# Kernel tuning notes

Measured on AMD Instinct MI355X. Metric: run time of the kernel, lower is better.

Reference implementation:

```python
import jax, jax.numpy as jnp
import numpy as np

N = 100000       # num nodes
E = 3200000      # train message edges (avg degree 32)
EP = 1600000     # pos (and neg) decode edges
F_IN = 128       # node feature dim
H1, H2 = 50, 10  # GCN layer widths from source


def setup_inputs() -> dict:
    key = jax.random.key(0)
    ks = jax.random.split(key, 6)
    x = jax.random.normal(ks[0], (N, F_IN), dtype=jnp.float32)
    train_pos_edge_index = jax.random.randint(ks[1], (2, E), 0, N)
    pos_edge_index = jax.random.randint(ks[2], (2, EP), 0, N)
    neg_edge_index = jax.random.randint(ks[3], (2, EP), 0, N)
    W1 = jax.random.normal(ks[4], (F_IN, H1), dtype=jnp.float32) / np.float32(np.sqrt(F_IN))
    b1 = jnp.zeros((H1,), jnp.float32)
    W2 = jax.random.normal(ks[5], (H1, H2), dtype=jnp.float32) / np.float32(np.sqrt(H1))
    b2 = jnp.zeros((H2,), jnp.float32)
    return {"x": x, "W1": W1, "b1": b1, "W2": W2, "b2": b2,
            "train_pos_edge_index": train_pos_edge_index,
            "pos_edge_index": pos_edge_index,
            "neg_edge_index": neg_edge_index}


def gcn_conv(x, W, b, src, dst, num_nodes):
    # x: [N, Fin] -> transform first (PyG GCNConv), then normalize+aggregate.
    h = x @ W                                                        # [N, Fout]
    deg = jax.ops.segment_sum(jnp.ones(src.shape, h.dtype), dst,
                              num_segments=num_nodes)                # in-degree incl self-loops
    dinv = jnp.where(deg > 0, jax.lax.rsqrt(deg), 0.0)
    norm = dinv[src] * dinv[dst]                                     # [E']
    msgs = h[src] * norm[:, None]                                    # gather + scale
    out = jax.ops.segment_sum(msgs, dst, num_segments=num_nodes)     # scatter-add
    return out + b


def reference(x, W1, b1, W2, b2, train_pos_edge_index, pos_edge_index, neg_edge_index):
    # GCNConv adds self-loops to the message edge set.
    loops = jnp.arange(N, dtype=train_pos_edge_index.dtype)
    src = jnp.concatenate([train_pos_edge_index[0], loops])
    dst = jnp.concatenate([train_pos_edge_index[1], loops])
    # encode(): conv1 -> relu -> conv2
    h = jax.nn.relu(gcn_conv(x, W1, b1, src, dst, N))                # [N, 50]
    z = gcn_conv(h, W2, b2, src, dst, N)                             # [N, 10]
    # decode(): concat pos/neg edges, edge-wise dot product of endpoint embeddings
    ei = jnp.concatenate([pos_edge_index, neg_edge_index], axis=-1)  # [2, 2*EP]
    logits = jnp.sum(z[ei[0]] * z[ei[1]], axis=-1)                   # [2*EP]
    return logits
```

## Files before the change

kernel.cpp:

```cpp
#include <hip/hip_runtime.h>

#define FIN 128
#define H1_ 50
#define H2_ 10

#define BKT_SHIFT 7
#define BKT_W 128
#define NB_MAX 800
#define P1_CHUNK 8192


__device__ inline float bf2f(unsigned int u16) {
    union { unsigned int i; float f; } c; c.i = u16 << 16; return c.f;
}
__device__ inline unsigned short f2bf(float f) {
    union { float f; unsigned int i; } c; c.f = f;
    unsigned int x = c.i;
    return (unsigned short)((x + 0x7FFFu + ((x >> 16) & 1u)) >> 16);
}


__global__ __launch_bounds__(256) void bucket_count(const int* __restrict__ dst,
                                                    int* __restrict__ bcnt, int E) {
    __shared__ int lh[NB_MAX];
    int tid = threadIdx.x;
    for (int i = tid; i < NB_MAX; i += 256) lh[i] = 0;
    __syncthreads();
    int lo = blockIdx.x * P1_CHUNK;
    int hi = min(lo + P1_CHUNK, E);
    for (int e = lo + tid; e < hi; e += 256)
        atomicAdd(&lh[dst[e] >> BKT_SHIFT], 1);
    __syncthreads();
    for (int b = tid; b < NB_MAX; b += 256) {
        int c = lh[b];
        if (c) atomicAdd(&bcnt[b], c);
    }
}

__global__ __launch_bounds__(256) void bucket_scan(const int* __restrict__ bcnt,
                                                   int* __restrict__ bbase,
                                                   int* __restrict__ bcursor,
                                                   int nb2, int E) {
    __shared__ int s[256];
    int t = threadIdx.x;
    int base = t * 4;
    int v0 = (base + 0 < nb2) ? bcnt[base + 0] : 0;
    int v1 = (base + 1 < nb2) ? bcnt[base + 1] : 0;
    int v2 = (base + 2 < nb2) ? bcnt[base + 2] : 0;
    int v3 = (base + 3 < nb2) ? bcnt[base + 3] : 0;
    int tsum = v0 + v1 + v2 + v3;
    s[t] = tsum;
    __syncthreads();
    for (int off = 1; off < 256; off <<= 1) {
        int x = (t >= off) ? s[t - off] : 0;
        __syncthreads();
        s[t] += x;
        __syncthreads();
    }
    int excl = s[t] - tsum;
    if (t == 0) bbase[nb2] = E;
    if (base + 0 < nb2) { bbase[base + 0] = excl; bcursor[base + 0] = excl; }
    excl += v0;
    if (base + 1 < nb2) { bbase[base + 1] = excl; bcursor[base + 1] = excl; }
    excl += v1;
    if (base + 2 < nb2) { bbase[base + 2] = excl; bcursor[base + 2] = excl; }
    excl += v2;
    if (base + 3 < nb2) { bbase[base + 3] = excl; bcursor[base + 3] = excl; }
}


__global__ __launch_bounds__(256) void partition_pass1(const int* __restrict__ src,
                                                       const int* __restrict__ dst,
                                                       int* __restrict__ bcursor,
                                                       int* __restrict__ pairbuf, int E) {
    __shared__ int lhist[NB_MAX];
    __shared__ int lbase[NB_MAX];
    int tid = threadIdx.x;
    for (int i = tid; i < NB_MAX; i += 256) lhist[i] = 0;
    __syncthreads();
    int lo = blockIdx.x * P1_CHUNK;
    int hi = min(lo + P1_CHUNK, E);
    for (int e = lo + tid; e < hi; e += 256)
        atomicAdd(&lhist[dst[e] >> BKT_SHIFT], 1);
    __syncthreads();
    for (int b = tid; b < NB_MAX; b += 256) {
        int c = lhist[b];
        lbase[b] = c ? atomicAdd(&bcursor[b], c) : 0;
    }
    __syncthreads();
    for (int i = tid; i < NB_MAX; i += 256) lhist[i] = 0;
    __syncthreads();
    for (int e = lo + tid; e < hi; e += 256) {
        int s = src[e], d = dst[e];
        int b = d >> BKT_SHIFT;
        int r = atomicAdd(&lhist[b], 1);
        pairbuf[lbase[b] + r] = s | ((d & (BKT_W - 1)) << 17);
    }
}


__global__ __launch_bounds__(256) void bucket_fill_scan(const int* __restrict__ pairbuf,
                                                        const int* __restrict__ bbase,
                                                        int* __restrict__ rowptr,
                                                        float* __restrict__ dinv,
                                                        int* __restrict__ ecol,
                                                        int N, int E) {
    __shared__ int cnt[BKT_W];
    __shared__ int sc[BKT_W];
    __shared__ int cur[BKT_W];
    int b = blockIdx.x;
    int base_node = b << BKT_SHIFT;
    int nnodes = min(BKT_W, N - base_node);
    int tid = threadIdx.x;
    if (tid < BKT_W) cnt[tid] = 0;
    __syncthreads();
    int lo = bbase[b], hi = bbase[b + 1];
    for (int j = lo + tid; j < hi; j += 256)
        atomicAdd(&cnt[pairbuf[j] >> 17], 1);
    __syncthreads();
    int c = (tid < BKT_W) ? cnt[tid] : 0;
    if (tid < BKT_W) sc[tid] = c;
    __syncthreads();
    for (int off = 1; off < BKT_W; off <<= 1) {
        int xv = (tid >= off && tid < BKT_W) ? sc[tid - off] : 0;
        __syncthreads();
        if (tid < BKT_W) sc[tid] += xv;
        __syncthreads();
    }
    if (tid < nnodes) {
        int rp = lo + sc[tid] - c;
        rowptr[base_node + tid] = rp;
        cur[tid] = rp;
        dinv[base_node + tid] = rsqrtf(1.0f + (float)c);
    }
    __syncthreads();
    for (int j = lo + tid; j < hi; j += 256) {
        int p = pairbuf[j];
        int pos = atomicAdd(&cur[p >> 17], 1);
        ecol[pos] = p & 0x1FFFF;
    }
    if (b == (int)gridDim.x - 1 && tid == 0) rowptr[N] = E;
}


#define G1_NODES 32
#define SX_PITCH 132
__global__ __launch_bounds__(256) void gemm1_kernel(const float* __restrict__ x,
                                                    const float* __restrict__ W1,
                                                    const float* __restrict__ dinv,
                                                    unsigned short* __restrict__ st1p, int N) {
    __shared__ float sW[FIN * 64];
    __shared__ float sX[G1_NODES * SX_PITCH];
    int tid = threadIdx.x;
    int nb = blockIdx.x * G1_NODES;
    for (int i = tid; i < FIN * 64; i += 256) {
        int k = i >> 6, f = i & 63;
        sW[i] = (f < H1_) ? W1[k * H1_ + f] : 0.0f;
    }
    {
        const float4* x4 = (const float4*)(x + (size_t)nb * FIN);
        for (int i = tid; i < G1_NODES * 32; i += 256) {
            int ln = i >> 5, kk = i & 31;
            float4 v = (nb + ln < N) ? x4[(size_t)ln * 32 + kk]
                                     : make_float4(0.f, 0.f, 0.f, 0.f);
            *(float4*)(&sX[ln * SX_PITCH + kk * 4]) = v;
        }
    }
    __syncthreads();
    int ln = tid >> 3;
    int g  = tid & 7;
    int node = nb + ln;
    const float* xr = &sX[ln * SX_PITCH];
    const float* wc = &sW[g * 8];
    float acc[8] = {0, 0, 0, 0, 0, 0, 0, 0};
#pragma unroll 4
    for (int k = 0; k < FIN; ++k) {
        float xv = xr[k];
        const float* w = &wc[k * 64];
#pragma unroll
        for (int j = 0; j < 8; ++j) acc[j] = fmaf(xv, w[j], acc[j]);
    }
    if (node >= N) return;
    float di = dinv[node];
    unsigned short o[8];
#pragma unroll
    for (int j = 0; j < 8; ++j) o[j] = f2bf(acc[j] * di);
    uint4 pk;
    pk.x = (unsigned)o[0] | ((unsigned)o[1] << 16);
    pk.y = (unsigned)o[2] | ((unsigned)o[3] << 16);
    pk.z = (unsigned)o[4] | ((unsigned)o[5] << 16);
    pk.w = (unsigned)o[6] | ((unsigned)o[7] << 16);
    *(uint4*)(st1p + (size_t)node * 64 + g * 8) = pk;
}


#define F2 25
__global__ __launch_bounds__(256) void csr_aggregate1(const unsigned short* __restrict__ st,
                                                      const int* __restrict__ rowptr,
                                                      const int* __restrict__ ecol,
                                                      const float* __restrict__ dinv,
                                                      const float* __restrict__ b,
                                                      float* __restrict__ out, int N) {
    int idx = blockIdx.x * blockDim.x + threadIdx.x;
    if (idx >= N * F2) return;
    int d  = idx / F2;
    int fp = idx - d * F2;
    int fo = 2 * fp;
    unsigned int self2 = *(const unsigned int*)(st + (size_t)d * 64 + fo);
    float acc0 = bf2f(self2 & 0xFFFFu);
    float acc1 = bf2f(self2 >> 16);
    int j = rowptr[d], end = rowptr[d + 1];
    for (; j + 3 < end; j += 4) {
        int s0 = ecol[j], s1 = ecol[j + 1], s2 = ecol[j + 2], s3 = ecol[j + 3];
        unsigned int v0 = *(const unsigned int*)(st + (size_t)s0 * 64 + fo);
        unsigned int v1 = *(const unsigned int*)(st + (size_t)s1 * 64 + fo);
        unsigned int v2 = *(const unsigned int*)(st + (size_t)s2 * 64 + fo);
        unsigned int v3 = *(const unsigned int*)(st + (size_t)s3 * 64 + fo);
        acc0 += (bf2f(v0 & 0xFFFFu) + bf2f(v1 & 0xFFFFu)) + (bf2f(v2 & 0xFFFFu) + bf2f(v3 & 0xFFFFu));
        acc1 += (bf2f(v0 >> 16) + bf2f(v1 >> 16)) + (bf2f(v2 >> 16) + bf2f(v3 >> 16));
    }
    for (; j < end; ++j) {
        unsigned int v = *(const unsigned int*)(st + (size_t)ecol[j] * 64 + fo);
        acc0 += bf2f(v & 0xFFFFu);
        acc1 += bf2f(v >> 16);
    }
    float vd = dinv[d];
    float r0 = fmaxf(fmaf(vd, acc0, b[fo]),     0.0f);
    float r1 = fmaxf(fmaf(vd, acc1, b[fo + 1]), 0.0f);
    *(float2*)(out + (size_t)d * H1_ + fo) = make_float2(r0, r1);
}


__global__ __launch_bounds__(256) void gemm2_kernel(const float* __restrict__ h,
                                                    const float* __restrict__ W2,
                                                    const float* __restrict__ dinv,
                                                    float* __restrict__ st2, int n) {
    __shared__ float sW[H1_ * H2_];
    int tid = threadIdx.x;
    for (int i = tid; i < H1_ * H2_; i += 256) sW[i] = W2[i];
    __syncthreads();
    int idx = blockIdx.x * blockDim.x + tid;
    if (idx >= n) return;
    int node = idx / H2_;
    int f    = idx - node * H2_;
    const float* hr = &h[node * H1_];
    float acc = 0.0f;
#pragma unroll
    for (int k = 0; k < H1_; ++k) acc = fmaf(hr[k], sW[k * H2_ + f], acc);
    st2[idx] = acc * dinv[node];
}


template <int F, bool RELU>
__global__ __launch_bounds__(256) void csr_aggregate(const float* __restrict__ st,
                                                     const int* __restrict__ rowptr,
                                                     const int* __restrict__ ecol,
                                                     const float* __restrict__ dinv,
                                                     const float* __restrict__ b,
                                                     float* __restrict__ out, int N) {
    int idx = blockIdx.x * blockDim.x + threadIdx.x;
    if (idx >= N * F) return;
    int d = idx / F;
    int f = idx - d * F;
    float acc = st[idx];
    int j = rowptr[d], end = rowptr[d + 1];
    for (; j + 3 < end; j += 4) {
        int s0 = ecol[j], s1 = ecol[j + 1], s2 = ecol[j + 2], s3 = ecol[j + 3];
        float a0 = st[s0 * F + f], a1 = st[s1 * F + f];
        float a2 = st[s2 * F + f], a3 = st[s3 * F + f];
        acc += (a0 + a1) + (a2 + a3);
    }
    for (; j < end; ++j) acc += st[ecol[j] * F + f];
    float v = fmaf(dinv[d], acc, b[f]);
    out[idx] = RELU ? fmaxf(v, 0.0f) : v;
}


__global__ void decode_kernel(const float* __restrict__ z, const int* __restrict__ pos,
                              const int* __restrict__ neg, float* __restrict__ logits, int EP) {
    int i = blockIdx.x * blockDim.x + threadIdx.x;
    if (i >= 2 * EP) return;
    int a, b;
    if (i < EP) { a = pos[i]; b = pos[EP + i]; }
    else        { int j = i - EP; a = neg[j]; b = neg[EP + j]; }
    const float* za = &z[a * H2_];
    const float* zb = &z[b * H2_];
    float acc = 0.0f;
#pragma unroll
    for (int f = 0; f < H2_; ++f) acc = fmaf(za[f], zb[f], acc);
    logits[i] = acc;
}


extern "C" void kernel_launch(void* const* d_in, const int* in_sizes, int n_in,
                              void* d_out, int out_size, void* d_ws, size_t ws_size,
                              hipStream_t stream) {
    const float* x   = (const float*)d_in[0];
    const float* W1  = (const float*)d_in[1];
    const float* b1  = (const float*)d_in[2];
    const float* W2  = (const float*)d_in[3];
    const float* b2  = (const float*)d_in[4];
    const int* train = (const int*)d_in[5];
    const int* pos   = (const int*)d_in[6];
    const int* neg   = (const int*)d_in[7];

    const int N  = in_sizes[0] / FIN;
    const int E  = in_sizes[5] / 2;
    const int EP = in_sizes[6] / 2;

    const int* tsrc = train;
    const int* tdst = train + E;

    size_t off = 0;
    int* rowptr   = (int*)d_ws;              off += (size_t)N + 1;
    int* bcnt     = (int*)d_ws + off;        off += NB_MAX;
    int* bbase    = (int*)d_ws + off;        off += NB_MAX + 1;
    int* bcursor  = (int*)d_ws + off;        off += NB_MAX;
    float* dinv   = (float*)d_ws + off;      off += N;
    off = (off + 3) & ~(size_t)3;
    float* regA   = (float*)d_ws + off;      off += (size_t)32 * N;
    float* regB   = (float*)d_ws + off;
    unsigned short* st1p = (unsigned short*)regA;
    float* st2    = regA;
    float* out2   = regA + (size_t)10 * N;
    float* out1   = regB;
    int* pairbuf  = (int*)regB;
    int* ecol     = (int*)d_out;
    float* logits = (float*)d_out;

    const int NB2 = (N + BKT_W - 1) >> BKT_SHIFT;
    const int P1B = (E + P1_CHUNK - 1) / P1_CHUNK;

    hipMemsetAsync(bcnt, 0, NB_MAX * sizeof(int), stream);
    bucket_count<<<P1B, 256, 0, stream>>>(tdst, bcnt, E);
    bucket_scan<<<1, 256, 0, stream>>>(bcnt, bbase, bcursor, NB2, E);
    partition_pass1<<<P1B, 256, 0, stream>>>(tsrc, tdst, bcursor, pairbuf, E);
    bucket_fill_scan<<<NB2, 256, 0, stream>>>(pairbuf, bbase, rowptr, dinv, ecol, N, E);

    gemm1_kernel<<<(N + G1_NODES - 1) / G1_NODES, 256, 0, stream>>>(x, W1, dinv, st1p, N);
    csr_aggregate1<<<(N * F2 + 255) / 256, 256, 0, stream>>>(
        st1p, rowptr, ecol, dinv, b1, out1, N);

    gemm2_kernel<<<(N * H2_ + 255) / 256, 256, 0, stream>>>(out1, W2, dinv, st2, N * H2_);
    csr_aggregate<H2_, false><<<(N * H2_ + 255) / 256, 256, 0, stream>>>(
        st2, rowptr, ecol, dinv, b2, out2, N);

    decode_kernel<<<(2 * EP + 255) / 256, 256, 0, stream>>>(out2, pos, neg, logits, EP);
}
```

Baseline: 476.4 us.

## Split edge partition into two-level radix pass via superbuckets

```diff
diff --git a/kernel.cpp b/kernel.cpp
--- a/kernel.cpp
+++ b/kernel.cpp
@@ -7,7 +7,11 @@
 #define BKT_SHIFT 7
 #define BKT_W 128
 #define NB_MAX 800
+#define SB_SHIFT 11
+#define SB_W 2048
+#define NSB_MAX 64
 #define P1_CHUNK 8192
+#define P1F_CHUNK 4096
 
 
 __device__ inline float bf2f(unsigned int u16) {
@@ -40,7 +44,9 @@
 __global__ __launch_bounds__(256) void bucket_scan(const int* __restrict__ bcnt,
                                                    int* __restrict__ bbase,
                                                    int* __restrict__ bcursor,
-                                                   int nb2, int E) {
+                                                   int* __restrict__ sbbase,
+                                                   int* __restrict__ sbcursor,
+                                                   int nb2, int nsb, int E) {
     __shared__ int s[256];
     int t = threadIdx.x;
     int base = t * 4;
@@ -66,35 +72,74 @@
     if (base + 2 < nb2) { bbase[base + 2] = excl; bcursor[base + 2] = excl; }
     excl += v2;
     if (base + 3 < nb2) { bbase[base + 3] = excl; bcursor[base + 3] = excl; }
-}
-
-
-__global__ __launch_bounds__(256) void partition_pass1(const int* __restrict__ src,
-                                                       const int* __restrict__ dst,
-                                                       int* __restrict__ bcursor,
-                                                       int* __restrict__ pairbuf, int E) {
-    __shared__ int lhist[NB_MAX];
-    __shared__ int lbase[NB_MAX];
-    int tid = threadIdx.x;
-    for (int i = tid; i < NB_MAX; i += 256) lhist[i] = 0;
+    __syncthreads();
+    if (t < nsb) {
+        int v = bbase[t * 16];
+        sbbase[t] = v;
+        sbcursor[t] = v;
+    }
+    if (t == 0) sbbase[nsb] = E;
+}
+
+
+__global__ __launch_bounds__(256) void partition_sb(const int* __restrict__ src,
+                                                    const int* __restrict__ dst,
+                                                    int* __restrict__ sbcursor,
+                                                    int* __restrict__ pairbuf1, int E) {
+    __shared__ int lh[NSB_MAX];
+    __shared__ int lb[NSB_MAX];
+    int tid = threadIdx.x;
+    if (tid < NSB_MAX) lh[tid] = 0;
     __syncthreads();
     int lo = blockIdx.x * P1_CHUNK;
     int hi = min(lo + P1_CHUNK, E);
     for (int e = lo + tid; e < hi; e += 256)
-        atomicAdd(&lhist[dst[e] >> BKT_SHIFT], 1);
-    __syncthreads();
-    for (int b = tid; b < NB_MAX; b += 256) {
-        int c = lhist[b];
-        lbase[b] = c ? atomicAdd(&bcursor[b], c) : 0;
-    }
-    __syncthreads();
-    for (int i = tid; i < NB_MAX; i += 256) lhist[i] = 0;
+        atomicAdd(&lh[dst[e] >> SB_SHIFT], 1);
+    __syncthreads();
+    if (tid < NSB_MAX) {
+        int c = lh[tid];
+        lb[tid] = c ? atomicAdd(&sbcursor[tid], c) : 0;
+        lh[tid] = 0;
+    }
     __syncthreads();
     for (int e = lo + tid; e < hi; e += 256) {
-        int s = src[e], d = dst[e];
-        int b = d >> BKT_SHIFT;
-        int r = atomicAdd(&lhist[b], 1);
-        pairbuf[lbase[b] + r] = s | ((d & (BKT_W - 1)) << 17);
+        int sv = src[e], d = dst[e];
+        int b = d >> SB_SHIFT;
+        int r = atomicAdd(&lh[b], 1);
+        pairbuf1[lb[b] + r] = sv | ((d & (SB_W - 1)) << 17);
+    }
+}
+
+
+__global__ __launch_bounds__(256) void partition_fine(const int* __restrict__ pairbuf1,
+                                                      const int* __restrict__ sbbase,
+                                                      int* __restrict__ bcursor,
+                                                      int* __restrict__ pairbuf2) {
+    int sb = blockIdx.y;
+    int seg_lo = sbbase[sb], seg_hi = sbbase[sb + 1];
+    int lo = seg_lo + blockIdx.x * P1F_CHUNK;
+    if (lo >= seg_hi) return;
+    int hi = min(lo + P1F_CHUNK, seg_hi);
+    __shared__ int lh[16];
+    __shared__ int lb[16];
+    int tid = threadIdx.x;
+    if (tid < 16) lh[tid] = 0;
+    __syncthreads();
+    for (int j = lo + tid; j < hi; j += 256)
+        atomicAdd(&lh[(pairbuf1[j] >> 17) >> BKT_SHIFT], 1);
+    __syncthreads();
+    if (tid < 16) {
+        int c = lh[tid];
+        lb[tid] = c ? atomicAdd(&bcursor[sb * 16 + tid], c) : 0;
+        lh[tid] = 0;
+    }
+    __syncthreads();
+    for (int j = lo + tid; j < hi; j += 256) {
+        int p = pairbuf1[j];
+        int din = p >> 17;
+        int fb = din >> BKT_SHIFT;
+        int r = atomicAdd(&lh[fb], 1);
+        pairbuf2[lb[fb] + r] = (p & 0x1FFFF) | ((din & (BKT_W - 1)) << 17);
     }
 }
 
@@ -316,26 +361,32 @@
     int* bcnt     = (int*)d_ws + off;        off += NB_MAX;
     int* bbase    = (int*)d_ws + off;        off += NB_MAX + 1;
     int* bcursor  = (int*)d_ws + off;        off += NB_MAX;
+    int* sbbase   = (int*)d_ws + off;        off += NSB_MAX + 1;
+    int* sbcursor = (int*)d_ws + off;        off += NSB_MAX;
     float* dinv   = (float*)d_ws + off;      off += N;
     off = (off + 3) & ~(size_t)3;
     float* regA   = (float*)d_ws + off;      off += (size_t)32 * N;
     float* regB   = (float*)d_ws + off;
+    int* pairbuf1 = (int*)regA;
     unsigned short* st1p = (unsigned short*)regA;
     float* st2    = regA;
     float* out2   = regA + (size_t)10 * N;
+    int* pairbuf2 = (int*)regB;
     float* out1   = regB;
-    int* pairbuf  = (int*)regB;
     int* ecol     = (int*)d_out;
     float* logits = (float*)d_out;
 
     const int NB2 = (N + BKT_W - 1) >> BKT_SHIFT;
+    const int NSB = (N + SB_W - 1) >> SB_SHIFT;
     const int P1B = (E + P1_CHUNK - 1) / P1_CHUNK;
+    int p1f_blocks = (2 * (E / NSB) + P1F_CHUNK - 1) / P1F_CHUNK + 1;
 
     hipMemsetAsync(bcnt, 0, NB_MAX * sizeof(int), stream);
     bucket_count<<<P1B, 256, 0, stream>>>(tdst, bcnt, E);
-    bucket_scan<<<1, 256, 0, stream>>>(bcnt, bbase, bcursor, NB2, E);
-    partition_pass1<<<P1B, 256, 0, stream>>>(tsrc, tdst, bcursor, pairbuf, E);
-    bucket_fill_scan<<<NB2, 256, 0, stream>>>(pairbuf, bbase, rowptr, dinv, ecol, N, E);
+    bucket_scan<<<1, 256, 0, stream>>>(bcnt, bbase, bcursor, sbbase, sbcursor, NB2, NSB, E);
+    partition_sb<<<P1B, 256, 0, stream>>>(tsrc, tdst, sbcursor, pairbuf1, E);
+    partition_fine<<<dim3(p1f_blocks, NSB), 256, 0, stream>>>(pairbuf1, sbbase, bcursor, pairbuf2);
+    bucket_fill_scan<<<NB2, 256, 0, stream>>>(pairbuf2, bbase, rowptr, dinv, ecol, N, E);
 
     gemm1_kernel<<<(N + G1_NODES - 1) / G1_NODES, 256, 0, stream>>>(x, W1, dinv, st1p, N);
     csr_aggregate1<<<(N * F2 + 255) / 256, 256, 0, stream>>>(
```

Result: faster. 451.7 us (-5.2%).
